# Kernel tuning notes

Hardware: AMD Instinct MI355X
Metric: run time of the kernel (lower is better)

Reference implementation:

```python
import jax, jax.numpy as jnp
import numpy as np

N, NFEAT, NHID, NHID2 = 10000, 512, 256, 128


def setup_inputs() -> dict:
    key = jax.random.key(0)
    k1, k2, k3, k4 = jax.random.split(key, 4)
    x = jax.random.normal(k1, (N, NFEAT), dtype=jnp.float32)
    # sparse-ish row-normalized adjacency, stored dense (as the module's spmm operand)
    raw = jax.random.uniform(k2, (N, N), dtype=jnp.float32)
    adj = jnp.where(raw > 0.995, raw, 0.0)
    adj = adj / jnp.maximum(adj.sum(axis=1, keepdims=True), 1e-6)
    W1 = jax.random.normal(k3, (NFEAT, NHID), dtype=jnp.float32) / np.sqrt(NFEAT)
    b1 = jnp.zeros((NHID,), dtype=jnp.float32)
    W2 = jax.random.normal(k4, (NHID, NHID2), dtype=jnp.float32) / np.sqrt(NHID)
    b2 = jnp.zeros((NHID2,), dtype=jnp.float32)
    return {"x": x, "adj": adj, "W1": W1, "b1": b1, "W2": W2, "b2": b2}


def gcn_conv(x, adj, W, b):
    # standard Kipf GCNConv: adj @ (x @ W) + b
    return adj @ (x @ W) + b


def reference(x, adj, W1, b1, W2, b2):
    h = jax.nn.relu(gcn_conv(x, adj, W1, b1))
    # dropout is identity in inference mode (training=False)
    h = jax.nn.relu(gcn_conv(h, adj, W2, b2))
    return h
```

## Files before the change

kernel.cpp:

```cpp
#include <hip/hip_runtime.h>

#define N_NODES 10000
#define NFEAT   512
#define NHID    256
#define NHID2   128
#define CAP     128

typedef __attribute__((ext_vector_type(8))) short bf16x8;
typedef __attribute__((ext_vector_type(4))) float f32x4;
typedef __attribute__((ext_vector_type(2))) int   i32x2;

__device__ __forceinline__ ushort f2bf(float f){
  union { float f; unsigned u; } v; v.f = f;
  unsigned r = v.u + 0x7FFFu + ((v.u >> 16) & 1u);
  return (ushort)(r >> 16);
}
__device__ __forceinline__ float bf2f(ushort u){
  union { unsigned u; float f; } v; v.u = ((unsigned)u) << 16; return v.f;
}

__global__ void k_cvt(const float* __restrict__ x, const float* __restrict__ W1,
                      const float* __restrict__ W2, ushort* __restrict__ xb,
                      ushort* __restrict__ w1t, ushort* __restrict__ w2t){
  const int b = blockIdx.x, t = threadIdx.x;
  if (b < 5000){
    int i = (b * 256 + t) * 4;
    float4 q = *(const float4*)(x + i);
    ushort4 o; o.x = f2bf(q.x); o.y = f2bf(q.y); o.z = f2bf(q.z); o.w = f2bf(q.w);
    *(ushort4*)(xb + i) = o;
  } else if (b < 5512){
    int id = (b - 5000) * 256 + t;
    int n = id >> 9, k = id & 511;
    w1t[id] = f2bf(W1[k * NHID + n]);
  } else {
    int id = (b - 5512) * 256 + t;
    int n = id >> 8, k = id & 255;
    w2t[id] = f2bf(W2[k * NHID2 + n]);
  }
}

__launch_bounds__(256)
__global__ void k_scan_gemm1(const float* __restrict__ adj, const ushort* __restrict__ xb,
                             const ushort* __restrict__ w1t, ushort* __restrict__ xw1_lo,
                             ushort* __restrict__ xw1_hi, int* __restrict__ row_nnz,
                             i32x2* __restrict__ pja){
  const int b = blockIdx.x, t = threadIdx.x;
  const int lane = t & 63, w = t >> 6;

  if (b < 628){
    const int bx = b % 157, by = b / 157;
    const int wr = w >> 1, wc = w & 1;
    const int r16 = lane & 15, kg = lane >> 4;
    const int row0 = bx * 64 + wr * 32;
    const int col0 = by * 64 + wc * 32;

    int arow[2], bcol[2];
    #pragma unroll
    for (int r = 0; r < 2; r++){
      int ar = row0 + r * 16 + r16;
      arow[r] = (ar >= N_NODES) ? (N_NODES - 1) : ar;
    }
    #pragma unroll
    for (int c = 0; c < 2; c++) bcol[c] = col0 + c * 16 + r16;

    f32x4 acc[2][2];
    #pragma unroll
    for (int r = 0; r < 2; r++)
      #pragma unroll
      for (int c = 0; c < 2; c++)
        acc[r][c] = (f32x4){0.f, 0.f, 0.f, 0.f};

    bf16x8 aA[2], bA[2], aB[2], bB[2];
    auto LOADF = [&](bf16x8* a, bf16x8* bb, int k0){
      #pragma unroll
      for (int r = 0; r < 2; r++)
        a[r] = *(const bf16x8*)(xb + (size_t)arow[r] * NFEAT + k0 + kg * 8);
      #pragma unroll
      for (int c = 0; c < 2; c++)
        bb[c] = *(const bf16x8*)(w1t + (size_t)bcol[c] * NFEAT + k0 + kg * 8);
    };
    auto MM = [&](bf16x8* a, bf16x8* bb){
      #pragma unroll
      for (int r = 0; r < 2; r++)
        #pragma unroll
        for (int c = 0; c < 2; c++)
          acc[r][c] = __builtin_amdgcn_mfma_f32_16x16x32_bf16(a[r], bb[c], acc[r][c], 0, 0, 0);
    };

    LOADF(aA, bA, 0);
    #pragma unroll
    for (int k0 = 0; k0 < NFEAT; k0 += 64){
      if (k0 + 32 < NFEAT) LOADF(aB, bB, k0 + 32);
      MM(aA, bA);
      if (k0 + 64 < NFEAT) LOADF(aA, bA, k0 + 64);
      if (k0 + 32 < NFEAT) MM(aB, bB);
    }

    ushort* dst = (by < 2) ? xw1_lo : xw1_hi;
    const int cbase = (by < 2) ? 0 : 128;
    #pragma unroll
    for (int r = 0; r < 2; r++)
      #pragma unroll
      for (int c = 0; c < 2; c++){
        int col = col0 + c * 16 + r16 - cbase;
        #pragma unroll
        for (int i = 0; i < 4; i++){
          int row = row0 + r * 16 + kg * 4 + i;
          if (row < N_NODES) dst[(size_t)row * 128 + col] = f2bf(acc[r][c][i]);
        }
      }
    return;
  }

  const int r = b - 628;
  const float* row = adj + (size_t)r * N_NODES;
  __shared__ int swave[4];

  f32x4 vals[10];
  #pragma unroll
  for (int v = 0; v < 9; v++)
    vals[v] = __builtin_nontemporal_load((const f32x4*)(row + v * 1024 + t * 4));
  vals[9] = (f32x4){0.f, 0.f, 0.f, 0.f};
  if (t < 196) vals[9] = __builtin_nontemporal_load((const f32x4*)(row + 9216 + t * 4));

  int cnt = 0;
  #pragma unroll
  for (int v = 0; v < 10; v++)
    cnt += (vals[v].x != 0.f) + (vals[v].y != 0.f) + (vals[v].z != 0.f) + (vals[v].w != 0.f);

  int incl = cnt;
  #pragma unroll
  for (int d = 1; d < 64; d <<= 1){
    int u = __shfl_up(incl, d, 64);
    if (lane >= d) incl += u;
  }
  if (lane == 63) swave[w] = incl;
  __syncthreads();
  int woff = 0, total = 0;
  #pragma unroll
  for (int i = 0; i < 4; i++){
    int s = swave[i];
    total += s;
    if (i < w) woff += s;
  }
  int pos = woff + incl - cnt;

  #pragma unroll
  for (int v = 0; v < 10; v++){
    float q[4] = {vals[v].x, vals[v].y, vals[v].z, vals[v].w};
    #pragma unroll
    for (int e = 0; e < 4; e++){
      if (q[e] != 0.f && pos < CAP){
        pja[(size_t)r * CAP + pos] = (i32x2){v * 1024 + t * 4 + e, __float_as_int(q[e])};
        pos++;
      }
    }
  }
  if (t == 0) row_nnz[r] = min(total, CAP);
}

template<bool TO_BF16, int DS>
__launch_bounds__(256)
__global__ void k_agg_half(const int* __restrict__ row_nnz, const i32x2* __restrict__ pja,
                           const ushort* __restrict__ table, const float* __restrict__ bias,
                           void* __restrict__ dst){
  const int r = blockIdx.x, t = threadIdx.x;
  __shared__ int   lj[CAP];
  __shared__ float la[CAP];
  __shared__ float part[16 * 128];
  const int n = row_nnz[r];
  if (t < n){
    i32x2 p = __builtin_nontemporal_load(pja + (size_t)r * CAP + t);
    lj[t] = p.x; la[t] = __int_as_float(p.y);
  }
  __syncthreads();

  const int slot = t >> 4, l16 = t & 15;
  float accv[8] = {0.f,0.f,0.f,0.f,0.f,0.f,0.f,0.f};
  for (int k = slot; k < n; k += 16){
    bf16x8 rv = *(const bf16x8*)(table + (size_t)lj[k] * 128 + l16 * 8);
    float a = la[k];
    #pragma unroll
    for (int j = 0; j < 8; j++)
      accv[j] += a * bf2f((ushort)rv[j]);
  }
  #pragma unroll
  for (int j = 0; j < 8; j++)
    part[slot * 128 + l16 * 8 + j] = accv[j];
  __syncthreads();

  if (t < 128){
    float s = 0.f;
    #pragma unroll
    for (int i = 0; i < 16; i++)
      s += part[i * 128 + t];
    s = fmaxf(s + bias[t], 0.f);
    if (TO_BF16) ((ushort*)dst)[(size_t)r * DS + t] = f2bf(s);
    else         ((float*) dst)[(size_t)r * DS + t] = s;
  }
}

__launch_bounds__(256)
__global__ void k_gemm2(const ushort* __restrict__ A, const ushort* __restrict__ Bt,
                        ushort* __restrict__ C){
  const int lane = threadIdx.x & 63;
  const int w    = threadIdx.x >> 6;
  const int wr   = w >> 1, wc = w & 1;
  const int r16  = lane & 15;
  const int kg   = lane >> 4;
  const int row0 = blockIdx.x * 64 + wr * 32;
  const int col0 = blockIdx.y * 64 + wc * 32;

  int arow[2], bcol[2];
  #pragma unroll
  for (int r = 0; r < 2; r++){
    int ar = row0 + r * 16 + r16;
    arow[r] = (ar >= N_NODES) ? (N_NODES - 1) : ar;
  }
  #pragma unroll
  for (int c = 0; c < 2; c++) bcol[c] = col0 + c * 16 + r16;

  f32x4 acc[2][2];
  #pragma unroll
  for (int r = 0; r < 2; r++)
    #pragma unroll
    for (int c = 0; c < 2; c++)
      acc[r][c] = (f32x4){0.f, 0.f, 0.f, 0.f};

  bf16x8 aA[2], bA[2], aB[2], bB[2];
  auto LOADF = [&](bf16x8* a, bf16x8* bb, int k0){
    #pragma unroll
    for (int r = 0; r < 2; r++)
      a[r] = *(const bf16x8*)(A + (size_t)arow[r] * NHID + k0 + kg * 8);
    #pragma unroll
    for (int c = 0; c < 2; c++)
      bb[c] = *(const bf16x8*)(Bt + (size_t)bcol[c] * NHID + k0 + kg * 8);
  };
  auto MM = [&](bf16x8* a, bf16x8* bb){
    #pragma unroll
    for (int r = 0; r < 2; r++)
      #pragma unroll
      for (int c = 0; c < 2; c++)
        acc[r][c] = __builtin_amdgcn_mfma_f32_16x16x32_bf16(a[r], bb[c], acc[r][c], 0, 0, 0);
  };

  LOADF(aA, bA, 0);
  #pragma unroll
  for (int k0 = 0; k0 < NHID; k0 += 64){
    if (k0 + 32 < NHID) LOADF(aB, bB, k0 + 32);
    MM(aA, bA);
    if (k0 + 64 < NHID) LOADF(aA, bA, k0 + 64);
    if (k0 + 32 < NHID) MM(aB, bB);
  }

  #pragma unroll
  for (int r = 0; r < 2; r++)
    #pragma unroll
    for (int c = 0; c < 2; c++){
      int col = col0 + c * 16 + r16;
      #pragma unroll
      for (int i = 0; i < 4; i++){
        int row = row0 + r * 16 + kg * 4 + i;
        if (row < N_NODES) C[(size_t)row * NHID2 + col] = f2bf(acc[r][c][i]);
      }
    }
}

extern "C" void kernel_launch(void* const* d_in, const int* in_sizes, int n_in,
                              void* d_out, int out_size, void* d_ws, size_t ws_size,
                              hipStream_t stream){
  const float* x   = (const float*)d_in[0];
  const float* adj = (const float*)d_in[1];
  const float* W1  = (const float*)d_in[2];
  const float* b1  = (const float*)d_in[3];
  const float* W2  = (const float*)d_in[4];
  const float* b2  = (const float*)d_in[5];
  float* out = (float*)d_out;
  char*  ws  = (char*)d_ws;

  ushort* xb     = (ushort*)(ws);
  ushort* w1t    = (ushort*)(ws + 10240000);
  ushort* w2t    = (ushort*)(ws + 10502144);
  ushort* xw1_lo = (ushort*)(ws + 10567680);
  ushort* xw1_hi = (ushort*)(ws + 13127680);
  ushort* Hb     = (ushort*)(ws + 15687680);
  ushort* hw2b   = (ushort*)(ws + 20807680);
  int*    nnz    = (int*)(ws + 23367680);
  i32x2*  pja    = (i32x2*)(ws + 23407680);

  k_cvt<<<5640, 256, 0, stream>>>(x, W1, W2, xb, w1t, w2t);

  k_scan_gemm1<<<10628, 256, 0, stream>>>(adj, xb, w1t, xw1_lo, xw1_hi, nnz, pja);

  k_agg_half<true, NHID><<<N_NODES, 256, 0, stream>>>(nnz, pja, xw1_lo, b1,       Hb);
  k_agg_half<true, NHID><<<N_NODES, 256, 0, stream>>>(nnz, pja, xw1_hi, b1 + 128, Hb + 128);

  k_gemm2<<<dim3(157, 2), 256, 0, stream>>>(Hb, w2t, hw2b);

  k_agg_half<false, NHID2><<<N_NODES, 256, 0, stream>>>(nnz, pja, hw2b, b2, out);
}
```

Baseline: 154.2 us.

## Restructure SpMM aggregation to one wave per row with batched row blocks

Rewrites the sparse aggregation kernels so each wavefront owns a whole output row, reading 4-byte bf16 pairs per lane instead of splitting neighbors over 16 slots and reducing through shared memory. Each block stages the sparse lists of 16 (or 8) rows into LDS, the two layer-1 half launches merge into one, and column indices are pre-shifted to byte offsets. This removes the shared-memory partial-sum reduction, extra syncs and per-row launch overhead. The cost is serial per-row neighbor loops with less memory-level parallelism, and staging of full CAP entries regardless of nnz.

```diff
diff --git a/kernel.cpp b/kernel.cpp
--- a/kernel.cpp
+++ b/kernel.cpp
@@ -151,7 +151,7 @@
     #pragma unroll
     for (int e = 0; e < 4; e++){
       if (q[e] != 0.f && pos < CAP){
-        pja[(size_t)r * CAP + pos] = (i32x2){v * 1024 + t * 4 + e, __float_as_int(q[e])};
+        pja[(size_t)r * CAP + pos] = (i32x2){(v * 1024 + t * 4 + e) << 8, __float_as_int(q[e])};
         pos++;
       }
     }
@@ -159,44 +159,42 @@
   if (t == 0) row_nnz[r] = min(total, CAP);
 }
 
-template<bool TO_BF16, int DS>
 __launch_bounds__(256)
-__global__ void k_agg_half(const int* __restrict__ row_nnz, const i32x2* __restrict__ pja,
-                           const ushort* __restrict__ table, const float* __restrict__ bias,
-                           void* __restrict__ dst){
-  const int r = blockIdx.x, t = threadIdx.x;
-  __shared__ int   lj[CAP];
-  __shared__ float la[CAP];
-  __shared__ float part[16 * 128];
-  const int n = row_nnz[r];
-  if (t < n){
-    i32x2 p = __builtin_nontemporal_load(pja + (size_t)r * CAP + t);
-    lj[t] = p.x; la[t] = __int_as_float(p.y);
+__global__ void k_agg1(const int* __restrict__ row_nnz, const i32x2* __restrict__ pja,
+                       const ushort* __restrict__ xw1_lo, const ushort* __restrict__ xw1_hi,
+                       const float* __restrict__ b1, ushort* __restrict__ Hb){
+  const int half = blockIdx.x & 1;
+  const int r0   = (blockIdx.x >> 1) * 16;
+  const int t = threadIdx.x;
+  __shared__ i32x2 sl[16][CAP];
+  __shared__ int   sn[16];
+  if (t < 16) sn[t] = row_nnz[r0 + t];
+  #pragma unroll
+  for (int e = 0; e < 8; e++){
+    int idx = t + e * 256;
+    int rr = idx >> 7, kk = idx & (CAP - 1);
+    sl[rr][kk] = pja[(size_t)(r0 + rr) * CAP + kk];
   }
   __syncthreads();
 
-  const int slot = t >> 4, l16 = t & 15;
-  float accv[8] = {0.f,0.f,0.f,0.f,0.f,0.f,0.f,0.f};
-  for (int k = slot; k < n; k += 16){
-    bf16x8 rv = *(const bf16x8*)(table + (size_t)lj[k] * 128 + l16 * 8);
-    float a = la[k];
-    #pragma unroll
-    for (int j = 0; j < 8; j++)
-      accv[j] += a * bf2f((ushort)rv[j]);
-  }
-  #pragma unroll
-  for (int j = 0; j < 8; j++)
-    part[slot * 128 + l16 * 8 + j] = accv[j];
-  __syncthreads();
-
-  if (t < 128){
-    float s = 0.f;
-    #pragma unroll
-    for (int i = 0; i < 16; i++)
-      s += part[i * 128 + t];
-    s = fmaxf(s + bias[t], 0.f);
-    if (TO_BF16) ((ushort*)dst)[(size_t)r * DS + t] = f2bf(s);
-    else         ((float*) dst)[(size_t)r * DS + t] = s;
+  const int wv = t >> 6, lane = t & 63;
+  const char* table = (const char*)(half ? xw1_hi : xw1_lo);
+  const float bias0 = b1[half * 128 + lane * 2 + 0];
+  const float bias1 = b1[half * 128 + lane * 2 + 1];
+
+  #pragma unroll
+  for (int rr = wv; rr < 16; rr += 4){
+    const int n = sn[rr];
+    float a0 = 0.f, a1 = 0.f;
+    for (int k = 0; k < n; k++){
+      i32x2 p = sl[rr][k];
+      uint pk = *(const uint*)(table + p.x + lane * 4);
+      float a = __int_as_float(p.y);
+      a0 += a * bf2f((ushort)(pk & 0xffff));
+      a1 += a * bf2f((ushort)(pk >> 16));
+    }
+    uint o = ((uint)f2bf(fmaxf(a1 + bias1, 0.f)) << 16) | (uint)f2bf(fmaxf(a0 + bias0, 0.f));
+    *(uint*)(Hb + (size_t)(r0 + rr) * NHID + half * 128 + lane * 2) = o;
   }
 }
 
@@ -264,6 +262,44 @@
         if (row < N_NODES) C[(size_t)row * NHID2 + col] = f2bf(acc[r][c][i]);
       }
     }
+}
+
+__launch_bounds__(256)
+__global__ void k_agg2(const int* __restrict__ row_nnz, const i32x2* __restrict__ pja,
+                       const ushort* __restrict__ hw2b, const float* __restrict__ b2,
+                       float* __restrict__ out){
+  const int r0 = blockIdx.x * 8;
+  const int t = threadIdx.x;
+  __shared__ i32x2 sl[8][CAP];
+  __shared__ int   sn[8];
+  if (t < 8) sn[t] = row_nnz[r0 + t];
+  #pragma unroll
+  for (int e = 0; e < 4; e++){
+    int idx = t + e * 256;
+    int rr = idx >> 7, kk = idx & (CAP - 1);
+    sl[rr][kk] = pja[(size_t)(r0 + rr) * CAP + kk];
+  }
+  __syncthreads();
+
+  const int wv = t >> 6, lane = t & 63;
+  const char* table = (const char*)hw2b;
+  const float bias0 = b2[lane * 2 + 0];
+  const float bias1 = b2[lane * 2 + 1];
+
+  #pragma unroll
+  for (int rr = wv; rr < 8; rr += 4){
+    const int n = sn[rr];
+    float a0 = 0.f, a1 = 0.f;
+    for (int k = 0; k < n; k++){
+      i32x2 p = sl[rr][k];
+      uint pk = *(const uint*)(table + p.x + lane * 4);
+      float a = __int_as_float(p.y);
+      a0 += a * bf2f((ushort)(pk & 0xffff));
+      a1 += a * bf2f((ushort)(pk >> 16));
+    }
+    float2 o = make_float2(fmaxf(a0 + bias0, 0.f), fmaxf(a1 + bias1, 0.f));
+    *(float2*)(out + (size_t)(r0 + rr) * NHID2 + lane * 2) = o;
+  }
 }
 
 extern "C" void kernel_launch(void* const* d_in, const int* in_sizes, int n_in,
@@ -292,10 +328,9 @@
 
   k_scan_gemm1<<<10628, 256, 0, stream>>>(adj, xb, w1t, xw1_lo, xw1_hi, nnz, pja);
 
-  k_agg_half<true, NHID><<<N_NODES, 256, 0, stream>>>(nnz, pja, xw1_lo, b1,       Hb);
-  k_agg_half<true, NHID><<<N_NODES, 256, 0, stream>>>(nnz, pja, xw1_hi, b1 + 128, Hb + 128);
+  k_agg1<<<1250, 256, 0, stream>>>(nnz, pja, xw1_lo, xw1_hi, b1, Hb);
 
   k_gemm2<<<dim3(157, 2), 256, 0, stream>>>(Hb, w2t, hw2b);
 
-  k_agg_half<false, NHID2><<<N_NODES, 256, 0, stream>>>(nnz, pja, hw2b, b2, out);
-}
+  k_agg2<<<1250, 256, 0, stream>>>(nnz, pja, hw2b, b2, out);
+}
```

Result: faster. 142.3 us (-7.7%).
